# Kernel tuning notes

Measured on AMD Instinct MI355X. Metric: run time of the kernel, lower is better.

## Reference

```python
import jax, jax.numpy as jnp
import numpy as np


def gcn_conv(x, src, dst, W, b, n):
    """PyG-style GCNConv: x@W then sym-normalized aggregation with self-loops."""
    loop = jnp.arange(n, dtype=src.dtype)
    s = jnp.concatenate([src, loop])
    d = jnp.concatenate([dst, loop])
    deg = jax.ops.segment_sum(jnp.ones_like(s, dtype=x.dtype), d, num_segments=n)
    dinv = jnp.where(deg > 0, jax.lax.rsqrt(deg), 0.0)
    norm = dinv[s] * dinv[d]                      # [E+n]
    xw = x @ W                                    # [n, out]
    msg = xw[s] * norm[:, None]                   # gather + scale
    return jax.ops.segment_sum(msg, d, num_segments=n) + b


def seq_encode(x, w1, b1, w2, b2):
    h = jax.nn.relu(x @ w1 + b1)
    return jax.nn.relu(h @ w2 + b2)


def setup_inputs() -> dict:
    key = jax.random.key(0)
    ks = jax.random.split(key, 24)
    Np, Nd, Ep, Ed = 100000, 50000, 3200000, 1600000
    Pin, Din, Psd, Dsd, H, O = 128, 64, 1024, 512, 128, 1

    def glorot(k, shape):
        lim = float(np.sqrt(6.0 / (shape[0] + shape[1])))
        return jax.random.uniform(k, shape, jnp.float32, -lim, lim)

    inp = {
        "protein_x": jax.random.normal(ks[0], (Np, Pin), jnp.float32),
        "protein_edge_index": jax.random.randint(ks[1], (2, Ep), 0, Np, jnp.int64),
        "drug_x": jax.random.normal(ks[2], (Nd, Din), jnp.float32),
        "drug_edge_index": jax.random.randint(ks[3], (2, Ed), 0, Nd, jnp.int64),
        "protein_seq": jax.random.normal(ks[4], (Psd,), jnp.float32),
        "drug_seq": jax.random.normal(ks[5], (Dsd,), jnp.float32),
        "pc1_w": glorot(ks[6], (Pin, H)), "pc1_b": jnp.zeros((H,), jnp.float32),
        "pc2_w": glorot(ks[7], (H, H)), "pc2_b": jnp.zeros((H,), jnp.float32),
        "dc1_w": glorot(ks[8], (Din, H)), "dc1_b": jnp.zeros((H,), jnp.float32),
        "dc2_w": glorot(ks[9], (H, H)), "dc2_b": jnp.zeros((H,), jnp.float32),
        "ps_w1": glorot(ks[10], (Psd, H)), "ps_b1": jnp.zeros((H,), jnp.float32),
        "ps_w2": glorot(ks[11], (H, H)), "ps_b2": jnp.zeros((H,), jnp.float32),
        "ds_w1": glorot(ks[12], (Dsd, H)), "ds_b1": jnp.zeros((H,), jnp.float32),
        "ds_w2": glorot(ks[13], (H, H)), "ds_b2": jnp.zeros((H,), jnp.float32),
        "fc1_w": glorot(ks[14], (4 * H, H)), "fc1_b": jnp.zeros((H,), jnp.float32),
        "fc2_w": glorot(ks[15], (H, O)), "fc2_b": jnp.zeros((O,), jnp.float32),
    }
    return inp


def reference(protein_x, protein_edge_index, drug_x, drug_edge_index,
              protein_seq, drug_seq,
              pc1_w, pc1_b, pc2_w, pc2_b, dc1_w, dc1_b, dc2_w, dc2_b,
              ps_w1, ps_b1, ps_w2, ps_b2, ds_w1, ds_b1, ds_w2, ds_b2,
              fc1_w, fc1_b, fc2_w, fc2_b):
    Np = protein_x.shape[0]
    Nd = drug_x.shape[0]
    ps, pd = protein_edge_index[0], protein_edge_index[1]
    ds_, dd = drug_edge_index[0], drug_edge_index[1]

    p = jax.nn.relu(gcn_conv(protein_x, ps, pd, pc1_w, pc1_b, Np))
    p = jax.nn.relu(gcn_conv(p, ps, pd, pc2_w, pc2_b, Np))
    p = p.mean(axis=0)                            # [H]

    d = jax.nn.relu(gcn_conv(drug_x, ds_, dd, dc1_w, dc1_b, Nd))
    d = jax.nn.relu(gcn_conv(d, ds_, dd, dc2_w, dc2_b, Nd))
    d = d.mean(axis=0)                            # [H]

    pseq = seq_encode(protein_seq, ps_w1, ps_b1, ps_w2, ps_b2)
    dseq = seq_encode(drug_seq, ds_w1, ds_b1, ds_w2, ds_b2)

    comb = jnp.concatenate([p, d, pseq, dseq], axis=0)  # [4H]
    h = jax.nn.relu(comb @ fc1_w + fc1_b)
    return h @ fc2_w + fc2_b
```

## Files before the change

### kernel.cpp

```cpp
#include <hip/hip_runtime.h>
#include <cstdint>
#include <cstddef>


#define NCB 256
#define BSH 9
#define BW  512
#define MPP 1024
#define MPD 512
#define MLP_NB 64

typedef __attribute__((ext_vector_type(8))) _Float16 f16x8;
typedef __attribute__((ext_vector_type(2))) _Float16 f16x2;
typedef __attribute__((ext_vector_type(2))) float f32x2;
typedef __attribute__((ext_vector_type(4))) float f32x4;

static __device__ __forceinline__ unsigned short f2h(float f) {
    _Float16 h = (_Float16)f;
    return __builtin_bit_cast(unsigned short, h);
}
static __device__ __forceinline__ f16x2 u2h(unsigned u) {
    return __builtin_bit_cast(f16x2, u);
}

static __device__ __forceinline__ void acc8v(f32x2* a, unsigned u0, unsigned u1) {
    a[0] += __builtin_amdgcn_cvt_pk_f32_fp8((int)u0, false);
    a[1] += __builtin_amdgcn_cvt_pk_f32_fp8((int)u0, true);
    a[2] += __builtin_amdgcn_cvt_pk_f32_fp8((int)u1, false);
    a[3] += __builtin_amdgcn_cvt_pk_f32_fp8((int)u1, true);
}

static __device__ __forceinline__ void build_body(int blk, const int* __restrict__ src,
                                                  const int* __restrict__ dst, int E, int chunk,
                                                  int* __restrict__ gcur,
                                                  unsigned* __restrict__ ebuf, int cap) {
    __shared__ int h[256];
    __shared__ int base[256];
    __shared__ int lc[256];
    const int t = threadIdx.x;
    h[t] = 0; lc[t] = 0;
    __syncthreads();
    const int e0 = blk * chunk;
    const int e1 = min(E, e0 + chunk);
    for (int e = e0 + t; e < e1; e += 256) atomicAdd(&h[dst[e] >> BSH], 1);
    __syncthreads();
    base[t] = h[t] ? atomicAdd(&gcur[t], h[t]) : 0;
    __syncthreads();
    for (int e = e0 + t; e < e1; e += 256) {
        int d = dst[e];
        int b = d >> BSH;
        int p = atomicAdd(&lc[b], 1);
        ebuf[(size_t)b * cap + base[b] + p] = ((unsigned)src[e] << BSH) | (unsigned)(d & (BW - 1));
    }
}

__global__ __launch_bounds__(256) void csr_build2(const int* sp, const int* dp, int Ep_, int chp,
                                                  int* gcp, unsigned* ebp, int capp,
                                                  const int* sd, const int* dd, int Ed_, int chd,
                                                  int* gcd, unsigned* ebd, int capd) {
    int b = blockIdx.x;
    if (b < NCB) build_body(b, sp, dp, Ep_, chp, gcp, ebp, capp);
    else         build_body(b - NCB, sd, dd, Ed_, chd, gcd, ebd, capd);
}

static __device__ __forceinline__ void finish_body(int b, const unsigned* __restrict__ ebuf,
                                                   const int* __restrict__ cnt, int cap, int n,
                                                   int* __restrict__ rowptr,
                                                   int* __restrict__ rend,
                                                   float* __restrict__ dinv,
                                                   int* __restrict__ col) {
    __shared__ int hist[BW];
    __shared__ int cur[BW];
    __shared__ int sh[256];
    const int t = threadIdx.x;
    const int nb = b << BSH;
    const int w = min(BW, n - nb);
    const int rb = b * cap;
    const int re = rb + cnt[b];
    hist[2 * t] = 0; hist[2 * t + 1] = 0;
    __syncthreads();
    for (int i = rb + t; i < re; i += 256) atomicAdd(&hist[ebuf[i] & (BW - 1)], 1);
    __syncthreads();
    const int a0 = hist[2 * t], a1 = hist[2 * t + 1];
    if (2 * t     < w) dinv[nb + 2 * t]     = rsqrtf((float)(a0 + 1));
    if (2 * t + 1 < w) dinv[nb + 2 * t + 1] = rsqrtf((float)(a1 + 1));
    sh[t] = a0 + a1; __syncthreads();
    for (int off = 1; off < 256; off <<= 1) {
        int add = (t >= off) ? sh[t - off] : 0;
        __syncthreads(); sh[t] += add; __syncthreads();
    }
    int base = t ? sh[t - 1] : 0;
    const int p0 = rb + base, p1 = rb + base + a0;
    if (2 * t < w) {
        rowptr[nb + 2 * t] = p0;
        rend[nb + 2 * t]   = p1;
    }
    if (2 * t + 1 < w) {
        rowptr[nb + 2 * t + 1] = p1;
        rend[nb + 2 * t + 1]   = p1 + a1;
    }
    cur[2 * t] = p0; cur[2 * t + 1] = p1;
    __syncthreads();
    for (int i = rb + t; i < re; i += 256) {
        unsigned r = ebuf[i];
        int pos = atomicAdd(&cur[r & (BW - 1)], 1);
        col[pos] = (int)(r >> BSH);
    }
}

__global__ __launch_bounds__(256) void csr_finish2(const unsigned* ebp, const int* gcp, int capp,
                                                   int np_, int* rpp, int* rep, float* dvp,
                                                   int* clp, int nbkp,
                                                   const unsigned* ebd, const int* gcd, int capd,
                                                   int nd_, int* rpd, int* red, float* dvd,
                                                   int* cld) {
    int b = blockIdx.x;
    if (b < nbkp) finish_body(b, ebp, gcp, capp, np_, rpp, rep, dvp, clp);
    else          finish_body(b - nbkp, ebd, gcd, capd, nd_, rpd, red, dvd, cld);
}

template <int K, bool IN16>
static __device__ __forceinline__ void xw_body(_Float16* __restrict__ Wt,
                                               unsigned char* __restrict__ T8, int bid,
                                               const void* __restrict__ xv,
                                               const float* __restrict__ W,
                                               const float* __restrict__ dinv,
                                               uint4* __restrict__ out8, int n) {
    constexpr int CH = K / 8;
    constexpr int KS = K / 32;
    const int tid = threadIdx.x;

    for (int i = tid; i < 128 * CH; i += 256) {
        const int col = i / CH, ch = i % CH;
        f16x8 v;
        #pragma unroll
        for (int j = 0; j < 8; ++j) v[j] = (_Float16)W[(ch * 8 + j) * 128 + col];
        *(f16x8*)&Wt[(col * CH + (ch ^ (col & (CH - 1)))) * 8] = v;
    }
    __syncthreads();

    const int wv = tid >> 6, ln = tid & 63;
    const int r0 = bid * 64 + wv * 16;
    const int row = r0 + (ln & 15);
    const int kg = (ln >> 4) * 8;

    f16x8 a[KS];
    if (row < n) {
        if constexpr (IN16) {
            const unsigned short* xr = (const unsigned short*)xv + (size_t)row * K;
            #pragma unroll
            for (int ks = 0; ks < KS; ++ks)
                a[ks] = *(const f16x8*)&xr[ks * 32 + kg];
        } else {
            const float* xr = (const float*)xv + (size_t)row * K;
            #pragma unroll
            for (int ks = 0; ks < KS; ++ks) {
                float4 u0 = *(const float4*)&xr[ks * 32 + kg];
                float4 u1 = *(const float4*)&xr[ks * 32 + kg + 4];
                f16x8 v;
                v[0] = (_Float16)u0.x; v[1] = (_Float16)u0.y;
                v[2] = (_Float16)u0.z; v[3] = (_Float16)u0.w;
                v[4] = (_Float16)u1.x; v[5] = (_Float16)u1.y;
                v[6] = (_Float16)u1.z; v[7] = (_Float16)u1.w;
                a[ks] = v;
            }
        }
    } else {
        #pragma unroll
        for (int ks = 0; ks < KS; ++ks) {
            f16x8 v;
            #pragma unroll
            for (int j = 0; j < 8; ++j) v[j] = (_Float16)0.f;
            a[ks] = v;
        }
    }

    const int rw0l = wv * 16 + (ln >> 4) * 4;
    float dv[4];
    #pragma unroll
    for (int r = 0; r < 4; ++r) dv[r] = (bid * 64 + rw0l + r < n) ? dinv[bid * 64 + rw0l + r] : 0.f;

    const int cl = ln & 15;
    #pragma unroll
    for (int nt = 0; nt < 8; ++nt) {
        const int col = nt * 16 + cl;
        f32x4 c = {0.f, 0.f, 0.f, 0.f};
        #pragma unroll
        for (int ks = 0; ks < KS; ++ks) {
            const int ch = ks * 4 + (ln >> 4);
            f16x8 b = *(const f16x8*)&Wt[(col * CH + (ch ^ (col & (CH - 1)))) * 8];
            c = __builtin_amdgcn_mfma_f32_16x16x32_f16(a[ks], b, c, 0, 0, 0);
        }
        #pragma unroll
        for (int r = 0; r < 4; ++r) {
            int q = __builtin_amdgcn_cvt_pk_fp8_f32(c[r] * dv[r], 0.f, 0, false);
            T8[(rw0l + r) * 128 + col] = (unsigned char)q;
        }
    }
    __syncthreads();
    for (int i = tid; i < 512; i += 256) {
        const int lr = i >> 3, ch = i & 7;
        const int rr = bid * 64 + lr;
        if (rr < n) out8[(size_t)rr * 8 + ch] = *(const uint4*)&T8[lr * 128 + ch * 16];
    }
    __syncthreads();
}

__global__ __launch_bounds__(256) void xw1_fused(const float* xp, const float* Wp,
                                                 const float* dvp, uint4* op, int np_, int nbp,
                                                 const float* xd, const float* Wd,
                                                 const float* dvd, uint4* od, int nd_) {
    __shared__ _Float16 Wt[128 * 128];
    __shared__ unsigned char T8[64 * 128];
    int b = blockIdx.x;
    if (b < nbp) xw_body<128, false>(Wt, T8, b, xp, Wp, dvp, op, np_);
    else         xw_body<64,  false>(Wt, T8, b - nbp, xd, Wd, dvd, od, nd_);
}

__global__ __launch_bounds__(256) void xw2_fused(const unsigned short* xp, const float* Wp,
                                                 const float* dvp, uint4* op, int np_, int nbp,
                                                 const unsigned short* xd, const float* Wd,
                                                 const float* dvd, uint4* od, int nd_) {
    __shared__ _Float16 Wt[128 * 128];
    __shared__ unsigned char T8[64 * 128];
    int b = blockIdx.x;
    if (b < nbp) xw_body<128, true>(Wt, T8, b, xp, Wp, dvp, op, np_);
    else         xw_body<128, true>(Wt, T8, b - nbp, xd, Wd, dvd, od, nd_);
}

static __device__ __forceinline__ void agg_body(int bid, const char* __restrict__ tab,
                                                const int* __restrict__ rowptr,
                                                const int* __restrict__ rend,
                                                const float* __restrict__ dinv,
                                                const int* __restrict__ col,
                                                const float* __restrict__ bias,
                                                uint4* __restrict__ out, int n) {
    const int wv = threadIdx.x >> 6, ln = threadIdx.x & 63;
    const int d = bid * 4 + wv;
    if (d >= n) return;
    const int g = ln >> 4;
    const unsigned coff = (unsigned)(ln & 15) << 3;
    const int c = ln & 15;
    const int beg = rowptr[d], end = rend[d];

    f32x2 a[4], b[4];
    #pragma unroll
    for (int i = 0; i < 4; ++i) { a[i] = (f32x2){0.f, 0.f}; b[i] = (f32x2){0.f, 0.f}; }
    if (g == 0) {
        uint2 v = *(const uint2*)(tab + (((unsigned)d << 7) + coff));
        acc8v(a, v.x, v.y);
    }

    int j = beg;
    unsigned o0 = 0, o1 = 0;
    if (j + 8 <= end) {
        o0 = ((unsigned)col[j + g] << 7) + coff;
        o1 = ((unsigned)col[j + 4 + g] << 7) + coff;
    }
    for (; j + 16 <= end; j += 8) {
        uint2 v0 = *(const uint2*)(tab + o0);
        uint2 v1 = *(const uint2*)(tab + o1);
        o0 = ((unsigned)col[j + 8 + g] << 7) + coff;
        o1 = ((unsigned)col[j + 12 + g] << 7) + coff;
        acc8v(a, v0.x, v0.y);
        acc8v(b, v1.x, v1.y);
    }
    if (j + 8 <= end) {
        uint2 v0 = *(const uint2*)(tab + o0);
        uint2 v1 = *(const uint2*)(tab + o1);
        acc8v(a, v0.x, v0.y);
        acc8v(b, v1.x, v1.y);
        j += 8;
    }
    for (; j < end; j += 4) {
        int jj = j + g;
        unsigned o = ((unsigned)col[min(jj, end - 1)] << 7) + coff;
        uint2 v = *(const uint2*)(tab + o);
        if (jj < end) acc8v(b, v.x, v.y);
    }
    #pragma unroll
    for (int i = 0; i < 4; ++i) a[i] += b[i];

    float r[8];
    #pragma unroll
    for (int i = 0; i < 4; ++i) { r[2 * i] = a[i][0]; r[2 * i + 1] = a[i][1]; }
    #pragma unroll
    for (int i = 0; i < 8; ++i) r[i] += __shfl_xor(r[i], 16);
    #pragma unroll
    for (int i = 0; i < 8; ++i) r[i] += __shfl_xor(r[i], 32);

    if (g == 0) {
        const float dv = dinv[d];
        const float* bp = &bias[c * 8];
        uint4 o;
        o.x = (unsigned)f2h(fmaxf(fmaf(dv, r[0], bp[0]), 0.f))
            | ((unsigned)f2h(fmaxf(fmaf(dv, r[1], bp[1]), 0.f)) << 16);
        o.y = (unsigned)f2h(fmaxf(fmaf(dv, r[2], bp[2]), 0.f))
            | ((unsigned)f2h(fmaxf(fmaf(dv, r[3], bp[3]), 0.f)) << 16);
        o.z = (unsigned)f2h(fmaxf(fmaf(dv, r[4], bp[4]), 0.f))
            | ((unsigned)f2h(fmaxf(fmaf(dv, r[5], bp[5]), 0.f)) << 16);
        o.w = (unsigned)f2h(fmaxf(fmaf(dv, r[6], bp[6]), 0.f))
            | ((unsigned)f2h(fmaxf(fmaf(dv, r[7], bp[7]), 0.f)) << 16);
        out[(size_t)d * 16 + c] = o;
    }
}

__global__ __launch_bounds__(256) void agg_fused(const char* tp, const int* rpp, const int* rep,
                                                 const float* dvp, const int* clp, const float* bp,
                                                 uint4* op, int np_, int nwbp,
                                                 const char* td, const int* rpd, const int* red,
                                                 const float* dvd, const int* cld, const float* bd,
                                                 uint4* od, int nd_) {
    int b = blockIdx.x;
    if (b < nwbp) agg_body(b, tp, rpp, rep, dvp, clp, bp, op, np_);
    else          agg_body(b - nwbp, td, rpd, red, dvd, cld, bd, od, nd_);
}

static __device__ __forceinline__ void meanp_body(int bid, const uint4* __restrict__ h, int n,
                                                  int nblk, float* __restrict__ partial) {
    const int t = threadIdx.x;
    const int c = t & 15;
    const int rl = t >> 4;
    const int rpb = (n + nblk - 1) / nblk;
    const int r0 = bid * rpb, r1 = min(n, r0 + rpb);
    float acc[8] = {0.f, 0.f, 0.f, 0.f, 0.f, 0.f, 0.f, 0.f};
    for (int r = r0 + rl; r < r1; r += 16) {
        uint4 v = h[(size_t)r * 16 + c];
        f16x2 p;
        p = u2h(v.x); acc[0] += (float)p[0]; acc[1] += (float)p[1];
        p = u2h(v.y); acc[2] += (float)p[0]; acc[3] += (float)p[1];
        p = u2h(v.z); acc[4] += (float)p[0]; acc[5] += (float)p[1];
        p = u2h(v.w); acc[6] += (float)p[0]; acc[7] += (float)p[1];
    }
    __shared__ float sh[16][128];
    #pragma unroll
    for (int k = 0; k < 8; ++k) sh[rl][c * 8 + k] = acc[k];
    __syncthreads();
    if (t < 128) {
        float s = 0.f;
        #pragma unroll
        for (int i = 0; i < 16; ++i) s += sh[i][t];
        partial[(size_t)bid * 128 + t] = s;
    }
}

static __device__ __forceinline__ void l1_body(int bid, const float* __restrict__ in,
                                               const float* __restrict__ w1, int IN,
                                               float* __restrict__ partial) {
    const int t = threadIdx.x;
    const int f = t & 127;
    const int half = t >> 7;
    const int kpb = IN / MLP_NB;
    const int k0 = bid * kpb;
    float acc = 0.f;
    #pragma unroll 4
    for (int k = k0 + half; k < k0 + kpb; k += 2)
        acc = fmaf(in[k], w1[(size_t)k * 128 + f], acc);
    __shared__ float sh2[256];
    sh2[t] = acc; __syncthreads();
    if (half == 0) partial[bid * 128 + f] = sh2[f] + sh2[128 + f];
}

__global__ __launch_bounds__(256) void meansq_fused(const uint4* hp, int np_, float* pp,
                                                    const uint4* hd, int nd_, float* pd,
                                                    const float* inp, const float* w1p, int INp,
                                                    float* mp,
                                                    const float* ind, const float* w1d, int INd,
                                                    float* md) {
    int b = blockIdx.x;
    if      (b < MPP)                 meanp_body(b, hp, np_, MPP, pp);
    else if (b < MPP + MPD)           meanp_body(b - MPP, hd, nd_, MPD, pd);
    else if (b < MPP + MPD + MLP_NB)  l1_body(b - MPP - MPD, inp, w1p, INp, mp);
    else                              l1_body(b - MPP - MPD - MLP_NB, ind, w1d, INd, md);
}

static __device__ __forceinline__ void meanf_body(const float* __restrict__ partial, int nrows,
                                                  float inv_n, float* __restrict__ out) {
    const int t = threadIdx.x;
    const int c4 = (t & 31) * 4;
    float4 acc = make_float4(0.f, 0.f, 0.f, 0.f);
    for (int r = (t >> 5); r < nrows; r += 8) {
        float4 v = *(const float4*)&partial[(size_t)r * 128 + c4];
        acc.x += v.x; acc.y += v.y; acc.z += v.z; acc.w += v.w;
    }
    __shared__ float4 sh[256];
    sh[t] = acc; __syncthreads();
    for (int off = 128; off >= 32; off >>= 1) {
        if (t < off) {
            float4 a = sh[t], o = sh[t + off];
            a.x += o.x; a.y += o.y; a.z += o.z; a.w += o.w;
            sh[t] = a;
        }
        __syncthreads();
    }
    if (t < 32) {
        float4 a = sh[t];
        a.x *= inv_n; a.y *= inv_n; a.z *= inv_n; a.w *= inv_n;
        *(float4*)&out[c4] = a;
    }
}

static __device__ __forceinline__ void seqfin_body(const float* __restrict__ partial,
                                                   const float* __restrict__ b1,
                                                   const float* __restrict__ w2,
                                                   const float* __restrict__ b2,
                                                   float* __restrict__ out) {
    const int t = threadIdx.x;
    __shared__ float h[128];
    if (t < 128) {
        float s = 0.f;
        #pragma unroll 8
        for (int i = 0; i < MLP_NB; ++i) s += partial[i * 128 + t];
        h[t] = fmaxf(s + b1[t], 0.f);
    }
    __syncthreads();
    if (t < 128) {
        float acc = 0.f;
        #pragma unroll 8
        for (int k = 0; k < 128; ++k) acc = fmaf(h[k], w2[k * 128 + t], acc);
        out[t] = fmaxf(acc + b2[t], 0.f);
    }
}

__global__ __launch_bounds__(256) void finish_fused(const float* pp, float invp, float* omp,
                                                    const float* pd, float invd, float* omd,
                                                    const float* sp, const float* b1p,
                                                    const float* w2p, const float* b2p, float* osp,
                                                    const float* sd, const float* b1d,
                                                    const float* w2d, const float* b2d, float* osd) {
    const int b = blockIdx.x;
    if      (b == 0) meanf_body(pp, MPP, invp, omp);
    else if (b == 1) meanf_body(pd, MPD, invd, omd);
    else if (b == 2) seqfin_body(sp, b1p, w2p, b2p, osp);
    else             seqfin_body(sd, b1d, w2d, b2d, osd);
}

__global__ __launch_bounds__(256) void head_one(const float* pm, const float* dm,
                                                const float* ps, const float* ds2,
                                                const float* fc1w, const float* fc1b,
                                                const float* fc2w, const float* fc2b,
                                                float* out) {
    const int t = threadIdx.x;
    __shared__ float comb[512];
    if (t < 128) {
        comb[t] = pm[t]; comb[128 + t] = dm[t];
        comb[256 + t] = ps[t]; comb[384 + t] = ds2[t];
    }
    __syncthreads();
    const int f = t & 127, half = t >> 7;
    float acc = 0.f;
    const int kb = half * 256;
    #pragma unroll 8
    for (int k = kb; k < kb + 256; ++k)
        acc = fmaf(comb[k], fc1w[(size_t)k * 128 + f], acc);
    __shared__ float hs[256];
    hs[t] = acc; __syncthreads();
    __shared__ float red[128];
    if (t < 128) {
        float h = fmaxf(hs[t] + hs[128 + t] + fc1b[t], 0.f);
        red[t] = h * fc2w[t];
    }
    __syncthreads();
    for (int off = 64; off > 0; off >>= 1) {
        if (t < off) red[t] += red[t + off];
        __syncthreads();
    }
    if (t == 0) out[0] = red[0] + fc2b[0];
}

static inline size_t align_up(size_t x, size_t a) { return (x + a - 1) / a * a; }

extern "C" void kernel_launch(void* const* d_in, const int* in_sizes, int n_in,
                              void* d_out, int out_size, void* d_ws, size_t ws_size,
                              hipStream_t stream) {
    const float* px   = (const float*)d_in[0];
    const int*   pei  = (const int*)d_in[1];
    const float* dx   = (const float*)d_in[2];
    const int*   dei  = (const int*)d_in[3];
    const float* pseq = (const float*)d_in[4];
    const float* dseq = (const float*)d_in[5];
    const float* pc1w = (const float*)d_in[6];  const float* pc1b = (const float*)d_in[7];
    const float* pc2w = (const float*)d_in[8];  const float* pc2b = (const float*)d_in[9];
    const float* dc1w = (const float*)d_in[10]; const float* dc1b = (const float*)d_in[11];
    const float* dc2w = (const float*)d_in[12]; const float* dc2b = (const float*)d_in[13];
    const float* psw1 = (const float*)d_in[14]; const float* psb1 = (const float*)d_in[15];
    const float* psw2 = (const float*)d_in[16]; const float* psb2 = (const float*)d_in[17];
    const float* dsw1 = (const float*)d_in[18]; const float* dsb1 = (const float*)d_in[19];
    const float* dsw2 = (const float*)d_in[20]; const float* dsb2 = (const float*)d_in[21];
    const float* fc1w = (const float*)d_in[22]; const float* fc1b = (const float*)d_in[23];
    const float* fc2w = (const float*)d_in[24]; const float* fc2b = (const float*)d_in[25];

    const int Np = in_sizes[0] / 128, Ep = in_sizes[1] / 2;
    const int Nd = in_sizes[2] / 64,  Ed = in_sizes[3] / 2;
    const int Psd = in_sizes[4], Dsd = in_sizes[5];

    const int capP = (Ep / 256 + Ep / 2048 + 1024 + 63) & ~63;
    const int capD = (Ed / 256 + Ed / 2048 + 1024 + 63) & ~63;

    char* w = (char*)d_ws;
    size_t off = 0;
    auto carve = [&](size_t bytes) -> void* {
        void* p = w + off;
        off = align_up(off + bytes, 256);
        return p;
    };
    unsigned char* tab_p  = (unsigned char*)carve((size_t)Np * 128);
    unsigned short* buf_p = (unsigned short*)carve((size_t)Np * 128 * 2);
    unsigned char* tab_d  = (unsigned char*)carve((size_t)Nd * 128);
    unsigned short* buf_d = (unsigned short*)carve((size_t)Nd * 128 * 2);
    int*      col_p  = (int*)carve((size_t)256 * capP * 4);
    unsigned* ebuf_p = (unsigned*)carve((size_t)256 * capP * 4);
    int*      col_d  = (int*)carve((size_t)256 * capD * 4);
    unsigned* ebuf_d = (unsigned*)carve((size_t)256 * capD * 4);
    int*   gcur_p   = (int*)carve(256 * 4);
    int*   gcur_d   = (int*)carve(256 * 4);
    int*   rowptr_p = (int*)carve((size_t)Np * 4);
    int*   rend_p   = (int*)carve((size_t)Np * 4);
    int*   rowptr_d = (int*)carve((size_t)Nd * 4);
    int*   rend_d   = (int*)carve((size_t)Nd * 4);
    float* dinv_p   = (float*)carve((size_t)Np * 4);
    float* dinv_d   = (float*)carve((size_t)Nd * 4);
    float* part_p   = (float*)carve((size_t)MPP * 128 * 4);
    float* part_d   = (float*)carve((size_t)MPD * 128 * 4);
    float* mlpp_p   = (float*)carve((size_t)MLP_NB * 128 * 4);
    float* mlpp_d   = (float*)carve((size_t)MLP_NB * 128 * 4);
    float* pmean    = (float*)carve(512);
    float* dmean    = (float*)carve(512);
    float* pseqo    = (float*)carve(512);
    float* dseqo    = (float*)carve(512);
    (void)ws_size; (void)n_in; (void)out_size;

    const int* psrc = pei; const int* pdst = pei + Ep;
    const int* dsrc = dei; const int* ddst = dei + Ed;
    const int chp = (((Ep + NCB - 1) / NCB) + 255) & ~255;
    const int chd = (((Ed + NCB - 1) / NCB) + 255) & ~255;
    const int nbkp = (Np + BW - 1) >> BSH, nbkd = (Nd + BW - 1) >> BSH;
    const int nbp = (Np + 63) / 64, nbd = (Nd + 63) / 64;
    const int nwbp = (Np + 3) / 4, nwbd = (Nd + 3) / 4;

    hipMemsetAsync(gcur_p, 0, 512 * 4, stream);
    csr_build2<<<2 * NCB, 256, 0, stream>>>(psrc, pdst, Ep, chp, gcur_p, ebuf_p, capP,
                                            dsrc, ddst, Ed, chd, gcur_d, ebuf_d, capD);
    csr_finish2<<<nbkp + nbkd, 256, 0, stream>>>(ebuf_p, gcur_p, capP, Np, rowptr_p, rend_p,
                                                 dinv_p, col_p, nbkp,
                                                 ebuf_d, gcur_d, capD, Nd, rowptr_d, rend_d,
                                                 dinv_d, col_d);

    xw1_fused<<<nbp + nbd, 256, 0, stream>>>(px, pc1w, dinv_p, (uint4*)tab_p, Np, nbp,
                                             dx, dc1w, dinv_d, (uint4*)tab_d, Nd);
    agg_fused<<<nwbp + nwbd, 256, 0, stream>>>((const char*)tab_p, rowptr_p, rend_p, dinv_p,
                                               col_p, pc1b, (uint4*)buf_p, Np, nwbp,
                                               (const char*)tab_d, rowptr_d, rend_d, dinv_d,
                                               col_d, dc1b, (uint4*)buf_d, Nd);
    xw2_fused<<<nbp + nbd, 256, 0, stream>>>(buf_p, pc2w, dinv_p, (uint4*)tab_p, Np, nbp,
                                             buf_d, dc2w, dinv_d, (uint4*)tab_d, Nd);
    agg_fused<<<nwbp + nwbd, 256, 0, stream>>>((const char*)tab_p, rowptr_p, rend_p, dinv_p,
                                               col_p, pc2b, (uint4*)buf_p, Np, nwbp,
                                               (const char*)tab_d, rowptr_d, rend_d, dinv_d,
                                               col_d, dc2b, (uint4*)buf_d, Nd);
    meansq_fused<<<MPP + MPD + 2 * MLP_NB, 256, 0, stream>>>(
        (const uint4*)buf_p, Np, part_p, (const uint4*)buf_d, Nd, part_d,
        pseq, psw1, Psd, mlpp_p, dseq, dsw1, Dsd, mlpp_d);
    finish_fused<<<4, 256, 0, stream>>>(part_p, 1.0f / (float)Np, pmean,
                                        part_d, 1.0f / (float)Nd, dmean,
                                        mlpp_p, psb1, psw2, psb2, pseqo,
                                        mlpp_d, dsb1, dsw2, dsb2, dseqo);
    head_one<<<1, 256, 0, stream>>>(pmean, dmean, pseqo, dseqo, fc1w, fc1b, fc2w, fc2b,
                                    (float*)d_out);
}
```

Before: 494.8 us.

## Merge CSR build/finish and tail reductions into cooperative kernels with grid sync

Replaces the memset plus csr_build2/csr_finish2 pair with one cooperative kernel that zeroes the counters, builds, and finishes, separated by grid-wide syncs. The mean/seq-MLP/finish/head kernels become a single cooperative tail kernel, and the mean partial block counts are halved so the grid fits co-resident. The goal is to cut kernel launch and inter-kernel gap overhead. In exchange it pays for grid barriers, the finish phase uses only the 512 resident blocks, and most blocks sit idle through the later tail stages.

```diff
diff --git a/kernel.cpp b/kernel.cpp
--- a/kernel.cpp
+++ b/kernel.cpp
@@ -1,13 +1,16 @@
 #include <hip/hip_runtime.h>
+#include <hip/hip_cooperative_groups.h>
 #include <cstdint>
 #include <cstddef>
+
+namespace cg = cooperative_groups;
 
 
 #define NCB 256
 #define BSH 9
 #define BW  512
-#define MPP 1024
-#define MPD 512
+#define MPP 512
+#define MPD 256
 #define MLP_NB 64
 
 typedef __attribute__((ext_vector_type(8))) _Float16 f16x8;
@@ -52,15 +55,6 @@
         int p = atomicAdd(&lc[b], 1);
         ebuf[(size_t)b * cap + base[b] + p] = ((unsigned)src[e] << BSH) | (unsigned)(d & (BW - 1));
     }
-}
-
-__global__ __launch_bounds__(256) void csr_build2(const int* sp, const int* dp, int Ep_, int chp,
-                                                  int* gcp, unsigned* ebp, int capp,
-                                                  const int* sd, const int* dd, int Ed_, int chd,
-                                                  int* gcd, unsigned* ebd, int capd) {
-    int b = blockIdx.x;
-    if (b < NCB) build_body(b, sp, dp, Ep_, chp, gcp, ebp, capp);
-    else         build_body(b - NCB, sd, dd, Ed_, chd, gcd, ebd, capd);
 }
 
 static __device__ __forceinline__ void finish_body(int b, const unsigned* __restrict__ ebuf,
@@ -108,15 +102,27 @@
     }
 }
 
-__global__ __launch_bounds__(256) void csr_finish2(const unsigned* ebp, const int* gcp, int capp,
-                                                   int np_, int* rpp, int* rep, float* dvp,
-                                                   int* clp, int nbkp,
-                                                   const unsigned* ebd, const int* gcd, int capd,
-                                                   int nd_, int* rpd, int* red, float* dvd,
-                                                   int* cld) {
-    int b = blockIdx.x;
-    if (b < nbkp) finish_body(b, ebp, gcp, capp, np_, rpp, rep, dvp, clp);
-    else          finish_body(b - nbkp, ebd, gcd, capd, nd_, rpd, red, dvd, cld);
+struct CsrArgs {
+    const int *sp, *dp; int Ep, chp; int* gcp; unsigned* ebp; int capp;
+    int *rpp, *rep; float* dvp; int* clp; int np, nbkp;
+    const int *sd, *dd; int Ed, chd; int* gcd; unsigned* ebd; int capd;
+    int *rpd, *red; float* dvd; int* cld; int nd, nbkd;
+};
+
+__global__ __launch_bounds__(256) void csr_coop(CsrArgs A) {
+    cg::grid_group grid = cg::this_grid();
+    const int b = blockIdx.x;
+    const int t = threadIdx.x;
+    if (b == 0) A.gcp[t] = 0;
+    else if (b == 1) A.gcd[t] = 0;
+    grid.sync();
+    if (b < NCB) build_body(b, A.sp, A.dp, A.Ep, A.chp, A.gcp, A.ebp, A.capp);
+    else         build_body(b - NCB, A.sd, A.dd, A.Ed, A.chd, A.gcd, A.ebd, A.capd);
+    grid.sync();
+    if (b < A.nbkp)
+        finish_body(b, A.ebp, A.gcp, A.capp, A.np, A.rpp, A.rep, A.dvp, A.clp);
+    else if (b < A.nbkp + A.nbkd)
+        finish_body(b - A.nbkp, A.ebd, A.gcd, A.capd, A.nd, A.rpd, A.red, A.dvd, A.cld);
 }
 
 template <int K, bool IN16>
@@ -342,6 +348,7 @@
         for (int i = 0; i < 16; ++i) s += sh[i][t];
         partial[(size_t)bid * 128 + t] = s;
     }
+    __syncthreads();
 }
 
 static __device__ __forceinline__ void l1_body(int bid, const float* __restrict__ in,
@@ -359,19 +366,7 @@
     __shared__ float sh2[256];
     sh2[t] = acc; __syncthreads();
     if (half == 0) partial[bid * 128 + f] = sh2[f] + sh2[128 + f];
-}
-
-__global__ __launch_bounds__(256) void meansq_fused(const uint4* hp, int np_, float* pp,
-                                                    const uint4* hd, int nd_, float* pd,
-                                                    const float* inp, const float* w1p, int INp,
-                                                    float* mp,
-                                                    const float* ind, const float* w1d, int INd,
-                                                    float* md) {
-    int b = blockIdx.x;
-    if      (b < MPP)                 meanp_body(b, hp, np_, MPP, pp);
-    else if (b < MPP + MPD)           meanp_body(b - MPP, hd, nd_, MPD, pd);
-    else if (b < MPP + MPD + MLP_NB)  l1_body(b - MPP - MPD, inp, w1p, INp, mp);
-    else                              l1_body(b - MPP - MPD - MLP_NB, ind, w1d, INd, md);
+    __syncthreads();
 }
 
 static __device__ __forceinline__ void meanf_body(const float* __restrict__ partial, int nrows,
@@ -398,6 +393,7 @@
         a.x *= inv_n; a.y *= inv_n; a.z *= inv_n; a.w *= inv_n;
         *(float4*)&out[c4] = a;
     }
+    __syncthreads();
 }
 
 static __device__ __forceinline__ void seqfin_body(const float* __restrict__ partial,
@@ -420,26 +416,18 @@
         for (int k = 0; k < 128; ++k) acc = fmaf(h[k], w2[k * 128 + t], acc);
         out[t] = fmaxf(acc + b2[t], 0.f);
     }
-}
-
-__global__ __launch_bounds__(256) void finish_fused(const float* pp, float invp, float* omp,
-                                                    const float* pd, float invd, float* omd,
-                                                    const float* sp, const float* b1p,
-                                                    const float* w2p, const float* b2p, float* osp,
-                                                    const float* sd, const float* b1d,
-                                                    const float* w2d, const float* b2d, float* osd) {
-    const int b = blockIdx.x;
-    if      (b == 0) meanf_body(pp, MPP, invp, omp);
-    else if (b == 1) meanf_body(pd, MPD, invd, omd);
-    else if (b == 2) seqfin_body(sp, b1p, w2p, b2p, osp);
-    else             seqfin_body(sd, b1d, w2d, b2d, osd);
-}
-
-__global__ __launch_bounds__(256) void head_one(const float* pm, const float* dm,
-                                                const float* ps, const float* ds2,
-                                                const float* fc1w, const float* fc1b,
-                                                const float* fc2w, const float* fc2b,
-                                                float* out) {
+    __syncthreads();
+}
+
+static __device__ __forceinline__ void head_body(const float* __restrict__ pm,
+                                                 const float* __restrict__ dm,
+                                                 const float* __restrict__ ps,
+                                                 const float* __restrict__ ds2,
+                                                 const float* __restrict__ fc1w,
+                                                 const float* __restrict__ fc1b,
+                                                 const float* __restrict__ fc2w,
+                                                 const float* __restrict__ fc2b,
+                                                 float* __restrict__ out) {
     const int t = threadIdx.x;
     __shared__ float comb[512];
     if (t < 128) {
@@ -466,6 +454,34 @@
         __syncthreads();
     }
     if (t == 0) out[0] = red[0] + fc2b[0];
+}
+
+struct TailArgs {
+    const uint4* hp; int np; float* pp;
+    const uint4* hd; int nd; float* pd;
+    const float* pseq; const float* w1p; int Psd; float* mp;
+    const float* dseq; const float* w1d; int Dsd; float* md;
+    float invp; float* pmean; float invd; float* dmean;
+    const float *b1p, *w2p, *b2p; float* pseqo;
+    const float *b1d, *w2d, *b2d; float* dseqo;
+    const float *fc1w, *fc1b, *fc2w, *fc2b; float* out;
+};
+
+__global__ __launch_bounds__(256) void tail_coop(TailArgs A) {
+    cg::grid_group grid = cg::this_grid();
+    const int b = blockIdx.x;
+    if      (b < MPP)                 meanp_body(b, A.hp, A.np, MPP, A.pp);
+    else if (b < MPP + MPD)           meanp_body(b - MPP, A.hd, A.nd, MPD, A.pd);
+    else if (b < MPP + MPD + MLP_NB)  l1_body(b - MPP - MPD, A.pseq, A.w1p, A.Psd, A.mp);
+    else                              l1_body(b - MPP - MPD - MLP_NB, A.dseq, A.w1d, A.Dsd, A.md);
+    grid.sync();
+    if      (b == 0) meanf_body(A.pp, MPP, A.invp, A.pmean);
+    else if (b == 1) meanf_body(A.pd, MPD, A.invd, A.dmean);
+    else if (b == 2) seqfin_body(A.mp, A.b1p, A.w2p, A.b2p, A.pseqo);
+    else if (b == 3) seqfin_body(A.md, A.b1d, A.w2d, A.b2d, A.dseqo);
+    grid.sync();
+    if (b == 0) head_body(A.pmean, A.dmean, A.pseqo, A.dseqo,
+                          A.fc1w, A.fc1b, A.fc2w, A.fc2b, A.out);
 }
 
 static inline size_t align_up(size_t x, size_t a) { return (x + a - 1) / a * a; }
@@ -538,13 +554,19 @@
     const int nbp = (Np + 63) / 64, nbd = (Nd + 63) / 64;
     const int nwbp = (Np + 3) / 4, nwbd = (Nd + 3) / 4;
 
-    hipMemsetAsync(gcur_p, 0, 512 * 4, stream);
-    csr_build2<<<2 * NCB, 256, 0, stream>>>(psrc, pdst, Ep, chp, gcur_p, ebuf_p, capP,
-                                            dsrc, ddst, Ed, chd, gcur_d, ebuf_d, capD);
-    csr_finish2<<<nbkp + nbkd, 256, 0, stream>>>(ebuf_p, gcur_p, capP, Np, rowptr_p, rend_p,
-                                                 dinv_p, col_p, nbkp,
-                                                 ebuf_d, gcur_d, capD, Nd, rowptr_d, rend_d,
-                                                 dinv_d, col_d);
+    CsrArgs ca;
+    ca.sp = psrc; ca.dp = pdst; ca.Ep = Ep; ca.chp = chp;
+    ca.gcp = gcur_p; ca.ebp = ebuf_p; ca.capp = capP;
+    ca.rpp = rowptr_p; ca.rep = rend_p; ca.dvp = dinv_p; ca.clp = col_p;
+    ca.np = Np; ca.nbkp = nbkp;
+    ca.sd = dsrc; ca.dd = ddst; ca.Ed = Ed; ca.chd = chd;
+    ca.gcd = gcur_d; ca.ebd = ebuf_d; ca.capd = capD;
+    ca.rpd = rowptr_d; ca.red = rend_d; ca.dvd = dinv_d; ca.cld = col_d;
+    ca.nd = Nd; ca.nbkd = nbkd;
+    {
+        void* params[] = { &ca };
+        hipLaunchCooperativeKernel((void*)csr_coop, dim3(2 * NCB), dim3(256), params, 0, stream);
+    }
 
     xw1_fused<<<nbp + nbd, 256, 0, stream>>>(px, pc1w, dinv_p, (uint4*)tab_p, Np, nbp,
                                              dx, dc1w, dinv_d, (uint4*)tab_d, Nd);
@@ -558,13 +580,21 @@
                                                col_p, pc2b, (uint4*)buf_p, Np, nwbp,
                                                (const char*)tab_d, rowptr_d, rend_d, dinv_d,
                                                col_d, dc2b, (uint4*)buf_d, Nd);
-    meansq_fused<<<MPP + MPD + 2 * MLP_NB, 256, 0, stream>>>(
-        (const uint4*)buf_p, Np, part_p, (const uint4*)buf_d, Nd, part_d,
-        pseq, psw1, Psd, mlpp_p, dseq, dsw1, Dsd, mlpp_d);
-    finish_fused<<<4, 256, 0, stream>>>(part_p, 1.0f / (float)Np, pmean,
-                                        part_d, 1.0f / (float)Nd, dmean,
-                                        mlpp_p, psb1, psw2, psb2, pseqo,
-                                        mlpp_d, dsb1, dsw2, dsb2, dseqo);
-    head_one<<<1, 256, 0, stream>>>(pmean, dmean, pseqo, dseqo, fc1w, fc1b, fc2w, fc2b,
-                                    (float*)d_out);
-}
+
+    TailArgs ta;
+    ta.hp = (const uint4*)buf_p; ta.np = Np; ta.pp = part_p;
+    ta.hd = (const uint4*)buf_d; ta.nd = Nd; ta.pd = part_d;
+    ta.pseq = pseq; ta.w1p = psw1; ta.Psd = Psd; ta.mp = mlpp_p;
+    ta.dseq = dseq; ta.w1d = dsw1; ta.Dsd = Dsd; ta.md = mlpp_d;
+    ta.invp = 1.0f / (float)Np; ta.pmean = pmean;
+    ta.invd = 1.0f / (float)Nd; ta.dmean = dmean;
+    ta.b1p = psb1; ta.w2p = psw2; ta.b2p = psb2; ta.pseqo = pseqo;
+    ta.b1d = dsb1; ta.w2d = dsw2; ta.b2d = dsb2; ta.dseqo = dseqo;
+    ta.fc1w = fc1w; ta.fc1b = fc1b; ta.fc2w = fc2w; ta.fc2b = fc2b;
+    ta.out = (float*)d_out;
+    {
+        void* params[] = { &ta };
+        hipLaunchCooperativeKernel((void*)tail_coop, dim3(MPP + MPD + 2 * MLP_NB), dim3(256),
+                                   params, 0, stream);
+    }
+}
```

New measurement: 808.4 us. 63.4% more time.
